# Kernel tuning notes

Hardware: AMD Instinct MI355X
Metric: run time of the kernel (lower is better)

## Reference

```python
import jax, jax.numpy as jnp
import numpy as np

DIM = 1024
HEADS = 16
DIM_HEAD = 64
DIM_INNER = HEADS * DIM_HEAD
SCALE = DIM_HEAD ** -0.5


def rmsnorm(x, w):
    eps = jnp.asarray(jnp.finfo(x.dtype).eps, x.dtype)
    var = jnp.mean(jnp.square(x), axis=-1, keepdims=True)
    return x * jax.lax.rsqrt(var + eps) * w


def setup_inputs() -> dict:
    key = jax.random.key(0)
    ks = jax.random.split(key, 6)
    tokens = jax.random.normal(ks[0], (2, 2048, DIM), dtype=jnp.float32)
    norm_w = jnp.ones((DIM,), dtype=jnp.float32)
    Wq = jax.random.normal(ks[1], (DIM, DIM_INNER), dtype=jnp.float32) * 0.02
    Wkv = jax.random.normal(ks[2], (DIM, 2 * DIM_INNER), dtype=jnp.float32) * 0.02
    Wout = jax.random.normal(ks[3], (DIM_INNER, DIM), dtype=jnp.float32) * 0.02
    Wg = jax.random.normal(ks[4], (DIM, HEADS), dtype=jnp.float32) * 0.02
    return {"tokens": tokens, "norm_w": norm_w, "Wq": Wq, "Wkv": Wkv, "Wout": Wout, "Wg": Wg}


def reference(tokens, norm_w, Wq, Wkv, Wout, Wg):
    b, n, _ = tokens.shape
    x = rmsnorm(tokens, norm_w)                      # [b, n, dim]
    q = x @ Wq                                       # [b, n, h*d]
    kv = x @ Wkv                                     # self-attention: context = tokens
    k, v = jnp.split(kv, 2, axis=-1)

    def split_heads(t):
        return t.reshape(b, n, HEADS, DIM_HEAD).transpose(0, 2, 1, 3)  # [b, h, n, d]

    q, k, v = map(split_heads, (q, k, v))

    sim = jnp.einsum('bhid,bhjd->bhij', q, k) * SCALE  # [b, h, n, n]
    causal_mask = jnp.triu(jnp.ones((n, n), dtype=bool), k=1)
    sim = jnp.where(causal_mask, jnp.asarray(-jnp.finfo(sim.dtype).max, sim.dtype), sim)
    attn = jax.nn.softmax(sim, axis=-1)
    out = jnp.einsum('bhij,bhjd->bhid', attn, v)       # [b, h, n, d]

    gates = jax.nn.sigmoid(x @ Wg)                     # [b, n, h]
    gates = gates.transpose(0, 2, 1)[..., None]        # [b, h, n, 1]
    out = gates * out

    out = out.transpose(0, 2, 1, 3).reshape(b, n, DIM_INNER)  # merge heads
    return out @ Wout                                  # [b, n, dim]
```

## Files before the change

### kernel.cpp

```cpp
#include <hip/hip_runtime.h>
#include <hip/hip_bf16.h>
#include <math.h>

constexpr int BB = 2;
constexpr int NN = 2048;
constexpr int DM = 1024;
constexpr int NH = 16;
constexpr int HD = 64;
constexpr int DI = NH * HD;
constexpr int MT = BB * NN;
constexpr float SM_SCALE = 0.125f * 1.44269504089f;

typedef __attribute__((ext_vector_type(8))) short short8v;
typedef __attribute__((ext_vector_type(4))) float f32x4;

__device__ inline unsigned cvt_pk_bf16(float lo, float hi) {
  unsigned r;
  asm("v_cvt_pk_bf16_f32 %0, %1, %2" : "=v"(r) : "v"(lo), "v"(hi));
  return r;
}
__device__ inline void pl32_swap(unsigned& a, unsigned& b) {
  asm("v_permlane32_swap_b32 %0, %1" : "+v"(a), "+v"(b));
}
__device__ inline void pl16_swap(unsigned& a, unsigned& b) {
  asm("v_permlane16_swap_b32 %0, %1" : "+v"(a), "+v"(b));
}
__device__ __forceinline__ void gload16(const void* g, void* l) {
  __builtin_amdgcn_global_load_lds(
      (const __attribute__((address_space(1))) unsigned int*)g,
      (__attribute__((address_space(3))) unsigned int*)l, 16, 0, 0);
}

__global__ __launch_bounds__(256) void k_rmsnorm(const float* __restrict__ tokens,
                                                 const float* __restrict__ w,
                                                 float* __restrict__ x,
                                                 __hip_bfloat16* __restrict__ xb) {
  const int tok = blockIdx.x;
  const int t = threadIdx.x;
  float4 v = ((const float4*)(tokens + (size_t)tok * DM))[t];
  float ss = v.x * v.x + v.y * v.y + v.z * v.z + v.w * v.w;
#pragma unroll
  for (int m = 1; m < 64; m <<= 1) ss += __shfl_xor(ss, m, 64);
  __shared__ float red[4];
  if ((t & 63) == 0) red[t >> 6] = ss;
  __syncthreads();
  float tot = red[0] + red[1] + red[2] + red[3];
  float inv = rsqrtf(tot * (1.0f / DM) + 1.1920929e-7f);
  float4 wv = ((const float4*)w)[t];
  float4 o;
  o.x = v.x * inv * wv.x;
  o.y = v.y * inv * wv.y;
  o.z = v.z * inv * wv.z;
  o.w = v.w * inv * wv.w;
  ((float4*)(x + (size_t)tok * DM))[t] = o;
  uint2 pk = make_uint2(cvt_pk_bf16(o.x, o.y), cvt_pk_bf16(o.z, o.w));
  *(uint2*)(xb + (size_t)tok * DM + t * 4) = pk;
}

__global__ __launch_bounds__(256) void k_wtrans(const float* __restrict__ W,
                                                __hip_bfloat16* __restrict__ Wt, int N) {
  __shared__ float tile[32][33];
  const int t = threadIdx.x;
  const int c = t & 31, r8 = t >> 5;
  const int kb = blockIdx.y * 32, nb = blockIdx.x * 32;
#pragma unroll
  for (int i = 0; i < 4; i++)
    tile[r8 + i * 8][c] = W[(size_t)(kb + r8 + i * 8) * N + nb + c];
  __syncthreads();
#pragma unroll
  for (int i = 0; i < 4; i++)
    Wt[(size_t)(nb + r8 + i * 8) * DM + kb + c] = __float2bfloat16(tile[c][r8 + i * 8]);
}

template <int MODE>
__global__ __launch_bounds__(256) void k_mgemm(const __hip_bfloat16* __restrict__ A,
                                               const __hip_bfloat16* __restrict__ Bt,
                                               float* __restrict__ C,
                                               __hip_bfloat16* __restrict__ OK,
                                               __hip_bfloat16* __restrict__ OV, int Nc) {
  __shared__ __hip_bfloat16 As[128][32];
  __shared__ __hip_bfloat16 Bs[64][32];
  const int t = threadIdx.x, wid = t >> 6, lane = t & 63;
  const int lq = lane & 15, lg = lane >> 4;
  const int wr = wid >> 1, wc = wid & 1;
  const int m0 = blockIdx.y * 128, n0 = blockIdx.x * 64;
  const int srow = lane >> 2, scol = (lane & 3) * 8;

  const __hip_bfloat16* Ag = A + (size_t)(m0 + wid * 32 + srow) * DM + scol;
  const __hip_bfloat16* Bg = Bt + (size_t)(n0 + wid * 16 + srow) * DM + scol;

  f32x4 acc[4][2];
#pragma unroll
  for (int i = 0; i < 4; i++)
#pragma unroll
    for (int j = 0; j < 2; j++) acc[i][j] = (f32x4){0.f, 0.f, 0.f, 0.f};

  for (int k0 = 0; k0 < DM; k0 += 32) {
    __syncthreads();
    gload16(Ag + k0, &As[wid * 32][0]);
    gload16(Ag + 16 * DM + k0, &As[wid * 32 + 16][0]);
    gload16(Bg + k0, &Bs[wid * 16][0]);
    __syncthreads();
    short8v af[4], bf[2];
#pragma unroll
    for (int i = 0; i < 4; i++) af[i] = *(const short8v*)&As[wr * 64 + i * 16 + lq][lg * 8];
#pragma unroll
    for (int j = 0; j < 2; j++) bf[j] = *(const short8v*)&Bs[wc * 32 + j * 16 + lq][lg * 8];
#pragma unroll
    for (int i = 0; i < 4; i++)
#pragma unroll
      for (int j = 0; j < 2; j++)
        acc[i][j] = __builtin_amdgcn_mfma_f32_16x16x32_bf16(af[i], bf[j], acc[i][j], 0, 0, 0);
  }

#pragma unroll
  for (int i = 0; i < 4; i++) {
    const int mb = m0 + wr * 64 + i * 16 + lg * 4;
#pragma unroll
    for (int j = 0; j < 2; j++) {
      const int c = n0 + wc * 32 + j * 16 + lq;
      if (MODE == 0) {
#pragma unroll
        for (int r = 0; r < 4; r++) C[(size_t)(mb + r) * Nc + c] = acc[i][j][r];
      } else if (MODE == 1 || (MODE == 2 && c < DI)) {
        const int b = mb >> 11, nl = mb & (NN - 1);
        const int h = (c & (DI - 1)) >> 6, d = c & 63;
        __hip_bfloat16* dst = OK + ((size_t)(b * NH + h) * NN + nl) * HD + d;
#pragma unroll
        for (int r = 0; r < 4; r++) dst[(size_t)r * HD] = __float2bfloat16(acc[i][j][r]);
      } else {
        const int cd = c - DI;
        const int b = mb >> 11, nl = mb & (NN - 1);
        const int h = cd >> 6, d = cd & 63;
        uint2 pk = make_uint2(cvt_pk_bf16(acc[i][j][0], acc[i][j][1]),
                              cvt_pk_bf16(acc[i][j][2], acc[i][j][3]));
        *(uint2*)(OV + ((size_t)(b * NH + h) * HD + d) * NN + nl) = pk;
      }
    }
  }
}

__global__ __launch_bounds__(256) void k_gates(const float* __restrict__ x,
                                               const float* __restrict__ Wg,
                                               float* __restrict__ g) {
  const int tok = blockIdx.x * 16 + (threadIdx.x >> 4);
  const int h = threadIdx.x & 15;
  const float* xr = x + (size_t)tok * DM;
  float s = 0.f;
  for (int k = 0; k < DM; k += 4) {
    float4 xv = *(const float4*)(xr + k);
    s += xv.x * Wg[(k + 0) * NH + h];
    s += xv.y * Wg[(k + 1) * NH + h];
    s += xv.z * Wg[(k + 2) * NH + h];
    s += xv.w * Wg[(k + 3) * NH + h];
  }
  g[(size_t)tok * NH + h] = 1.f / (1.f + __expf(-s));
}

__global__ __launch_bounds__(64) void k_attn_mfma(const __hip_bfloat16* __restrict__ Qb,
                                                  const __hip_bfloat16* __restrict__ Kb,
                                                  const __hip_bfloat16* __restrict__ Vtb,
                                                  const float* __restrict__ gates,
                                                  __hip_bfloat16* __restrict__ aob,
                                                  float* __restrict__ Opart,
                                                  float* __restrict__ mpart,
                                                  float* __restrict__ lpart) {
  const int bid = blockIdx.x;
  const int xcd = bid & 7;
  const int s = bid >> 3;
  const int gq = s / 96;
  const int t = s % 96;
  const int bh = gq * 8 + xcd;
  const int i = t / 3, j = t % 3;
  int grp, kt0, kt1, chunk;
  if (j < 2) {
    grp = 63 - i;
    chunk = j;
    const int nt = (grp >> 1) + 1;
    const int h0 = (nt + 1) >> 1;
    kt0 = chunk ? h0 : 0;
    kt1 = chunk ? nt : h0;
  } else {
    grp = 31 - i;
    chunk = -1;
    kt0 = 0;
    kt1 = (grp >> 1) + 1;
  }
  const int lane = threadIdx.x;
  const int lg = lane >> 4, lq = lane & 15;
  const int q0 = grp * 32;

  const __hip_bfloat16* Qh = Qb + (size_t)bh * NN * HD;
  const __hip_bfloat16* Kh = Kb + (size_t)bh * NN * HD;
  const __hip_bfloat16* Vh = Vtb + (size_t)bh * HD * NN;

  short8v qf0[2], qf1[2];
#pragma unroll
  for (int ks = 0; ks < 2; ks++) {
    qf0[ks] = *(const short8v*)(Qh + (size_t)(q0 + lq) * HD + ks * 32 + lg * 8);
    qf1[ks] = *(const short8v*)(Qh + (size_t)(q0 + 16 + lq) * HD + ks * 32 + lg * 8);
  }

  f32x4 oacc0[4], oacc1[4];
#pragma unroll
  for (int jx = 0; jx < 4; jx++) {
    oacc0[jx] = (f32x4){0.f, 0.f, 0.f, 0.f};
    oacc1[jx] = (f32x4){0.f, 0.f, 0.f, 0.f};
  }
  float m0r = -3.0e38f, l0p = 0.f, m1r = -3.0e38f, l1p = 0.f;

  auto LOADK = [&](short8v (*kf)[2], int kt) {
    const int kvb = kt * 64;
#pragma unroll
    for (int jx = 0; jx < 4; jx++)
#pragma unroll
      for (int ks = 0; ks < 2; ks++)
        kf[jx][ks] = *(const short8v*)(Kh + (size_t)(kvb + jx * 16 + lq) * HD + ks * 32 + lg * 8);
  };
  auto LOADV = [&](short8v (*vf)[2], int kt) {
    const int kvb = kt * 64;
#pragma unroll
    for (int jx = 0; jx < 4; jx++)
#pragma unroll
      for (int ks = 0; ks < 2; ks++)
        vf[jx][ks] = *(const short8v*)(Vh + (size_t)(jx * 16 + lq) * NN + kvb + ks * 32 + lg * 8);
  };

  auto GROUP = [&](const short8v* qf, f32x4* oacc, float& m_run, float& l_part,
                   int q0g, const short8v (*kf)[2], const short8v (*vf)[2], int kt) {
    const int kvb = kt * 64;
    f32x4 sacc[4];
#pragma unroll
    for (int jx = 0; jx < 4; jx++) sacc[jx] = (f32x4){0.f, 0.f, 0.f, 0.f};
#pragma unroll
    for (int jx = 0; jx < 4; jx++)
#pragma unroll
      for (int ks = 0; ks < 2; ks++)
        sacc[jx] = __builtin_amdgcn_mfma_f32_16x16x32_bf16(kf[jx][ks], qf[ks], sacc[jx], 0, 0, 0);

    const int qg = q0g + lq;
    const bool diag = (kvb + 63 > q0g);
    float ss[4][4];
#pragma unroll
    for (int jx = 0; jx < 4; jx++)
#pragma unroll
      for (int r = 0; r < 4; r++) {
        float v = sacc[jx][r] * SM_SCALE;
        if (diag && (kvb + jx * 16 + lg * 4 + r > qg)) v = -3.0e38f;
        ss[jx][r] = v;
      }

    float tmax = -3.0e38f;
#pragma unroll
    for (int jx = 0; jx < 4; jx++)
#pragma unroll
      for (int r = 0; r < 4; r++) tmax = fmaxf(tmax, ss[jx][r]);

    if (!__all(tmax <= m_run + 8.0f)) {
      float tr = fmaxf(tmax, __shfl_xor(tmax, 16));
      tr = fmaxf(tr, __shfl_xor(tr, 32));
      const float mnew = fmaxf(m_run, tr);
      const float cf = exp2f(m_run - mnew);
      l_part *= cf;
#pragma unroll
      for (int jx = 0; jx < 4; jx++)
#pragma unroll
        for (int r = 0; r < 4; r++) oacc[jx][r] *= cf;
      m_run = mnew;
    }

    float psum = 0.f;
    unsigned upk[4], vpk[4];
#pragma unroll
    for (int jx = 0; jx < 4; jx++) {
      float p0 = exp2f(ss[jx][0] - m_run), p1 = exp2f(ss[jx][1] - m_run);
      float p2 = exp2f(ss[jx][2] - m_run), p3 = exp2f(ss[jx][3] - m_run);
      psum += (p0 + p1) + (p2 + p3);
      upk[jx] = cvt_pk_bf16(p0, p1);
      vpk[jx] = cvt_pk_bf16(p2, p3);
    }
    l_part += psum;

#pragma unroll
    for (int ks = 0; ks < 2; ks++) {
      unsigned w0 = upk[2 * ks], w2 = upk[2 * ks + 1];
      unsigned w1 = vpk[2 * ks], w3 = vpk[2 * ks + 1];
      pl32_swap(w0, w2);
      pl16_swap(w0, w2);
      pl32_swap(w1, w3);
      pl16_swap(w1, w3);
      int4 bw = make_int4((int)w0, (int)w1, (int)w2, (int)w3);
      short8v pb = __builtin_bit_cast(short8v, bw);
#pragma unroll
      for (int jx = 0; jx < 4; jx++)
        oacc[jx] = __builtin_amdgcn_mfma_f32_16x16x32_bf16(vf[jx][ks], pb, oacc[jx], 0, 0, 0);
    }
  };

  short8v kf[4][2], vf[4][2];
  for (int kt = kt0; kt < kt1; kt++) {
    LOADK(kf, kt);
    LOADV(vf, kt);
    GROUP(qf0, oacc0, m0r, l0p, q0, kf, vf, kt);
    GROUP(qf1, oacc1, m1r, l1p, q0 + 16, kf, vf, kt);
  }

  float l0 = l0p + __shfl_xor(l0p, 16);
  l0 += __shfl_xor(l0, 32);
  float l1 = l1p + __shfl_xor(l1p, 16);
  l1 += __shfl_xor(l1, 32);

  if (chunk >= 0) {
    const int gi = grp - 32;
    const size_t pidx = (size_t)(bh * 32 + gi) * 2 + chunk;
    float* Op = Opart + pidx * 2048;
#pragma unroll
    for (int jx = 0; jx < 4; jx++) {
      *(f32x4*)(Op + lq * 64 + jx * 16 + lg * 4) = oacc0[jx];
      *(f32x4*)(Op + (16 + lq) * 64 + jx * 16 + lg * 4) = oacc1[jx];
    }
    if (lane < 16) {
      mpart[pidx * 32 + lane] = m0r;
      mpart[pidx * 32 + 16 + lane] = m1r;
      lpart[pidx * 32 + lane] = l0;
      lpart[pidx * 32 + 16 + lane] = l1;
    }
    return;
  }

  const int b = bh >> 4, h = bh & 15;
  const float g0 = gates[((size_t)(b * NN + q0 + lq)) * NH + h];
  const float g1 = gates[((size_t)(b * NN + q0 + 16 + lq)) * NH + h];
  const float sc0 = g0 / l0, sc1 = g1 / l1;
  __shared__ float ots[32][68];
#pragma unroll
  for (int jx = 0; jx < 4; jx++)
#pragma unroll
    for (int r = 0; r < 4; r++) {
      ots[lq][jx * 16 + lg * 4 + r] = oacc0[jx][r] * sc0;
      ots[16 + lq][jx * 16 + lg * 4 + r] = oacc1[jx][r] * sc1;
    }
  __syncthreads();
  const int d0 = (lane & 3) * 16;
#pragma unroll
  for (int rr = 0; rr < 2; rr++) {
    const int rl = rr * 16 + (lane >> 2);
    __hip_bfloat16* aor = aob + ((size_t)(b * NN + q0 + rl)) * DI + h * HD + d0;
#pragma unroll
    for (int u = 0; u < 4; u++) {
      uint2 pk = make_uint2(
          cvt_pk_bf16(ots[rl][d0 + 4 * u + 0], ots[rl][d0 + 4 * u + 1]),
          cvt_pk_bf16(ots[rl][d0 + 4 * u + 2], ots[rl][d0 + 4 * u + 3]));
      *(uint2*)(aor + 4 * u) = pk;
    }
  }
}

__global__ __launch_bounds__(256) void k_attn_combine(const float* __restrict__ Opart,
                                                      const float* __restrict__ mpart,
                                                      const float* __restrict__ lpart,
                                                      const float* __restrict__ gates,
                                                      __hip_bfloat16* __restrict__ aob) {
  const int hg = blockIdx.x;
  const int h = hg >> 5, gi = hg & 31;
  const int grp = 32 + gi;
  const int t = threadIdx.x;
  const int row = t >> 3, dq = (t & 7) * 8;
  const size_t p0 = (size_t)hg * 2, p1 = p0 + 1;
  const float m0 = mpart[p0 * 32 + row], m1 = mpart[p1 * 32 + row];
  const float l0 = lpart[p0 * 32 + row], l1 = lpart[p1 * 32 + row];
  const float M = fmaxf(m0, m1);
  const float a0 = exp2f(m0 - M), a1 = exp2f(m1 - M);
  const float L = a0 * l0 + a1 * l1;
  const int b = h >> 4, hh = h & 15;
  const int grow = grp * 32 + row;
  const float sc = gates[((size_t)(b * NN + grow)) * NH + hh] / L;
  const float* O0 = Opart + p0 * 2048 + row * 64 + dq;
  const float* O1 = Opart + p1 * 2048 + row * 64 + dq;
  unsigned pk[4];
#pragma unroll
  for (int u = 0; u < 4; u++) {
    float x0 = (a0 * O0[2 * u + 0] + a1 * O1[2 * u + 0]) * sc;
    float x1 = (a0 * O0[2 * u + 1] + a1 * O1[2 * u + 1]) * sc;
    pk[u] = cvt_pk_bf16(x0, x1);
  }
  __hip_bfloat16* dst = aob + ((size_t)(b * NN + grow)) * DI + hh * 64 + dq;
  *(uint4*)dst = make_uint4(pk[0], pk[1], pk[2], pk[3]);
}

extern "C" void kernel_launch(void* const* d_in, const int* in_sizes, int n_in,
                              void* d_out, int out_size, void* d_ws, size_t ws_size,
                              hipStream_t stream) {
  const float* tokens = (const float*)d_in[0];
  const float* norm_w = (const float*)d_in[1];
  const float* Wq     = (const float*)d_in[2];
  const float* Wkv    = (const float*)d_in[3];
  const float* Wout   = (const float*)d_in[4];
  const float* Wg     = (const float*)d_in[5];
  float* out = (float*)d_out;

  float* ws = (float*)d_ws;
  float* x  = ws;
  float* gb = x + (size_t)MT * DM;
  __hip_bfloat16* xb   = (__hip_bfloat16*)(gb + (size_t)MT * NH);
  __hip_bfloat16* aob  = xb + (size_t)MT * DM;
  __hip_bfloat16* Qb   = aob + (size_t)MT * DM;
  __hip_bfloat16* Kb   = Qb + (size_t)MT * DI;
  __hip_bfloat16* Vtb  = Kb + (size_t)MT * DI;
  __hip_bfloat16* Wqt  = Vtb + (size_t)MT * DI;
  __hip_bfloat16* Wkvt = Wqt + (size_t)DI * DM;
  __hip_bfloat16* Woutt= Wkvt + (size_t)2 * DI * DM;
  float* Opart = (float*)(Woutt + (size_t)DM * DI);
  float* mpart = Opart + (size_t)2048 * 2048;
  float* lpart = mpart + (size_t)2048 * 32;

  k_rmsnorm<<<MT, 256, 0, stream>>>(tokens, norm_w, x, xb);
  k_wtrans<<<dim3(DI / 32, DM / 32), 256, 0, stream>>>(Wq, Wqt, DI);
  k_wtrans<<<dim3(2 * DI / 32, DM / 32), 256, 0, stream>>>(Wkv, Wkvt, 2 * DI);
  k_wtrans<<<dim3(DM / 32, DI / 32), 256, 0, stream>>>(Wout, Woutt, DM);
  k_gates<<<MT / 16, 256, 0, stream>>>(x, Wg, gb);
  k_mgemm<1><<<dim3(DI / 64, MT / 128), 256, 0, stream>>>(xb, Wqt, nullptr, Qb, nullptr, DI);
  k_mgemm<2><<<dim3(2 * DI / 64, MT / 128), 256, 0, stream>>>(xb, Wkvt, nullptr, Kb, Vtb, 2 * DI);
  k_attn_mfma<<<dim3(32 * 96), 64, 0, stream>>>(Qb, Kb, Vtb, gb, aob, Opart, mpart, lpart);
  k_attn_combine<<<dim3(1024), 256, 0, stream>>>(Opart, mpart, lpart, gb, aob);
  k_mgemm<0><<<dim3(DM / 64, MT / 128), 256, 0, stream>>>(aob, Woutt, out, nullptr, nullptr, DM);
}
```

Baseline: 203.2 us.

## Fuse gates into rmsnorm, merge weight transposes and Q/KV GEMMs

Computes the sigmoid gate projection inside the rmsnorm kernel from a shared-memory copy of the normalized row, removing the separate gates kernel and its re-read of x. The three weight-transpose launches become one kernel, and the Q and KV projections run as a single GEMM over a concatenated transposed weight. The goal is fewer launches and a fuller GEMM grid. In exchange, rmsnorm does more work per block and reads Wg with strided loads.

```diff
diff --git a/kernel.cpp b/kernel.cpp
--- a/kernel.cpp
+++ b/kernel.cpp
@@ -33,15 +33,19 @@
 
 __global__ __launch_bounds__(256) void k_rmsnorm(const float* __restrict__ tokens,
                                                  const float* __restrict__ w,
+                                                 const float* __restrict__ Wg,
                                                  float* __restrict__ x,
-                                                 __hip_bfloat16* __restrict__ xb) {
+                                                 __hip_bfloat16* __restrict__ xb,
+                                                 float* __restrict__ g) {
+  __shared__ float xs[DM];
+  __shared__ float red[4];
+  __shared__ float gred[4][16];
   const int tok = blockIdx.x;
   const int t = threadIdx.x;
   float4 v = ((const float4*)(tokens + (size_t)tok * DM))[t];
   float ss = v.x * v.x + v.y * v.y + v.z * v.z + v.w * v.w;
 #pragma unroll
   for (int m = 1; m < 64; m <<= 1) ss += __shfl_xor(ss, m, 64);
-  __shared__ float red[4];
   if ((t & 63) == 0) red[t >> 6] = ss;
   __syncthreads();
   float tot = red[0] + red[1] + red[2] + red[3];
@@ -55,27 +59,58 @@
   ((float4*)(x + (size_t)tok * DM))[t] = o;
   uint2 pk = make_uint2(cvt_pk_bf16(o.x, o.y), cvt_pk_bf16(o.z, o.w));
   *(uint2*)(xb + (size_t)tok * DM + t * 4) = pk;
-}
-
-__global__ __launch_bounds__(256) void k_wtrans(const float* __restrict__ W,
-                                                __hip_bfloat16* __restrict__ Wt, int N) {
+  *(float4*)&xs[t * 4] = o;
+  __syncthreads();
+  const int h = t & 15, seg = t >> 4, wid = t >> 6;
+  const float* xp = &xs[seg * 64];
+  const float* wp = Wg + (size_t)(seg * 64) * NH + h;
+  float s = 0.f;
+#pragma unroll 8
+  for (int k = 0; k < 64; k++) s = fmaf(xp[k], wp[(size_t)k * NH], s);
+  s += __shfl_xor(s, 16);
+  s += __shfl_xor(s, 32);
+  if ((t & 63) < 16) gred[wid][h] = s;
+  __syncthreads();
+  if (t < 16) {
+    float tot2 = gred[0][t] + gred[1][t] + gred[2][t] + gred[3][t];
+    g[(size_t)tok * NH + t] = 1.f / (1.f + __expf(-tot2));
+  }
+}
+
+__global__ __launch_bounds__(256) void k_wtrans_all(const float* __restrict__ Wq,
+                                                    const float* __restrict__ Wkv,
+                                                    const float* __restrict__ Wout,
+                                                    __hip_bfloat16* __restrict__ Wqkvt,
+                                                    __hip_bfloat16* __restrict__ Woutt) {
+  const int bx = blockIdx.x;
+  const int kb = blockIdx.y * 32;
+  const float* W;
+  __hip_bfloat16* dst;
+  int N, col0, drow0;
+  if (bx < 32) {
+    W = Wq; N = DI; col0 = bx * 32; dst = Wqkvt; drow0 = col0;
+  } else if (bx < 96) {
+    W = Wkv; N = 2 * DI; col0 = (bx - 32) * 32; dst = Wqkvt; drow0 = DI + col0;
+  } else {
+    W = Wout; N = DM; col0 = (bx - 96) * 32; dst = Woutt; drow0 = col0;
+  }
   __shared__ float tile[32][33];
   const int t = threadIdx.x;
   const int c = t & 31, r8 = t >> 5;
-  const int kb = blockIdx.y * 32, nb = blockIdx.x * 32;
 #pragma unroll
   for (int i = 0; i < 4; i++)
-    tile[r8 + i * 8][c] = W[(size_t)(kb + r8 + i * 8) * N + nb + c];
+    tile[r8 + i * 8][c] = W[(size_t)(kb + r8 + i * 8) * N + col0 + c];
   __syncthreads();
 #pragma unroll
   for (int i = 0; i < 4; i++)
-    Wt[(size_t)(nb + r8 + i * 8) * DM + kb + c] = __float2bfloat16(tile[c][r8 + i * 8]);
+    dst[(size_t)(drow0 + r8 + i * 8) * DM + kb + c] = __float2bfloat16(tile[c][r8 + i * 8]);
 }
 
 template <int MODE>
 __global__ __launch_bounds__(256) void k_mgemm(const __hip_bfloat16* __restrict__ A,
                                                const __hip_bfloat16* __restrict__ Bt,
                                                float* __restrict__ C,
+                                               __hip_bfloat16* __restrict__ OQ,
                                                __hip_bfloat16* __restrict__ OK,
                                                __hip_bfloat16* __restrict__ OV, int Nc) {
   __shared__ __hip_bfloat16 As[128][32];
@@ -122,39 +157,29 @@
       if (MODE == 0) {
 #pragma unroll
         for (int r = 0; r < 4; r++) C[(size_t)(mb + r) * Nc + c] = acc[i][j][r];
-      } else if (MODE == 1 || (MODE == 2 && c < DI)) {
+      } else {
         const int b = mb >> 11, nl = mb & (NN - 1);
-        const int h = (c & (DI - 1)) >> 6, d = c & 63;
-        __hip_bfloat16* dst = OK + ((size_t)(b * NH + h) * NN + nl) * HD + d;
-#pragma unroll
-        for (int r = 0; r < 4; r++) dst[(size_t)r * HD] = __float2bfloat16(acc[i][j][r]);
-      } else {
-        const int cd = c - DI;
-        const int b = mb >> 11, nl = mb & (NN - 1);
-        const int h = cd >> 6, d = cd & 63;
-        uint2 pk = make_uint2(cvt_pk_bf16(acc[i][j][0], acc[i][j][1]),
-                              cvt_pk_bf16(acc[i][j][2], acc[i][j][3]));
-        *(uint2*)(OV + ((size_t)(b * NH + h) * HD + d) * NN + nl) = pk;
+        if (c < DI) {
+          const int h = c >> 6, d = c & 63;
+          __hip_bfloat16* dst = OQ + ((size_t)(b * NH + h) * NN + nl) * HD + d;
+#pragma unroll
+          for (int r = 0; r < 4; r++) dst[(size_t)r * HD] = __float2bfloat16(acc[i][j][r]);
+        } else if (c < 2 * DI) {
+          const int ck = c - DI;
+          const int h = ck >> 6, d = ck & 63;
+          __hip_bfloat16* dst = OK + ((size_t)(b * NH + h) * NN + nl) * HD + d;
+#pragma unroll
+          for (int r = 0; r < 4; r++) dst[(size_t)r * HD] = __float2bfloat16(acc[i][j][r]);
+        } else {
+          const int cd = c - 2 * DI;
+          const int h = cd >> 6, d = cd & 63;
+          uint2 pk = make_uint2(cvt_pk_bf16(acc[i][j][0], acc[i][j][1]),
+                                cvt_pk_bf16(acc[i][j][2], acc[i][j][3]));
+          *(uint2*)(OV + ((size_t)(b * NH + h) * HD + d) * NN + nl) = pk;
+        }
       }
     }
   }
-}
-
-__global__ __launch_bounds__(256) void k_gates(const float* __restrict__ x,
-                                               const float* __restrict__ Wg,
-                                               float* __restrict__ g) {
-  const int tok = blockIdx.x * 16 + (threadIdx.x >> 4);
-  const int h = threadIdx.x & 15;
-  const float* xr = x + (size_t)tok * DM;
-  float s = 0.f;
-  for (int k = 0; k < DM; k += 4) {
-    float4 xv = *(const float4*)(xr + k);
-    s += xv.x * Wg[(k + 0) * NH + h];
-    s += xv.y * Wg[(k + 1) * NH + h];
-    s += xv.z * Wg[(k + 2) * NH + h];
-    s += xv.w * Wg[(k + 3) * NH + h];
-  }
-  g[(size_t)tok * NH + h] = 1.f / (1.f + __expf(-s));
 }
 
 __global__ __launch_bounds__(64) void k_attn_mfma(const __hip_bfloat16* __restrict__ Qb,
@@ -402,26 +427,23 @@
   float* ws = (float*)d_ws;
   float* x  = ws;
   float* gb = x + (size_t)MT * DM;
-  __hip_bfloat16* xb   = (__hip_bfloat16*)(gb + (size_t)MT * NH);
-  __hip_bfloat16* aob  = xb + (size_t)MT * DM;
-  __hip_bfloat16* Qb   = aob + (size_t)MT * DM;
-  __hip_bfloat16* Kb   = Qb + (size_t)MT * DI;
-  __hip_bfloat16* Vtb  = Kb + (size_t)MT * DI;
-  __hip_bfloat16* Wqt  = Vtb + (size_t)MT * DI;
-  __hip_bfloat16* Wkvt = Wqt + (size_t)DI * DM;
-  __hip_bfloat16* Woutt= Wkvt + (size_t)2 * DI * DM;
+  __hip_bfloat16* xb    = (__hip_bfloat16*)(gb + (size_t)MT * NH);
+  __hip_bfloat16* aob   = xb + (size_t)MT * DM;
+  __hip_bfloat16* Qb    = aob + (size_t)MT * DM;
+  __hip_bfloat16* Kb    = Qb + (size_t)MT * DI;
+  __hip_bfloat16* Vtb   = Kb + (size_t)MT * DI;
+  __hip_bfloat16* Wqkvt = Vtb + (size_t)MT * DI;
+  __hip_bfloat16* Woutt = Wqkvt + (size_t)3 * DI * DM;
   float* Opart = (float*)(Woutt + (size_t)DM * DI);
   float* mpart = Opart + (size_t)2048 * 2048;
   float* lpart = mpart + (size_t)2048 * 32;
 
-  k_rmsnorm<<<MT, 256, 0, stream>>>(tokens, norm_w, x, xb);
-  k_wtrans<<<dim3(DI / 32, DM / 32), 256, 0, stream>>>(Wq, Wqt, DI);
-  k_wtrans<<<dim3(2 * DI / 32, DM / 32), 256, 0, stream>>>(Wkv, Wkvt, 2 * DI);
-  k_wtrans<<<dim3(DM / 32, DI / 32), 256, 0, stream>>>(Wout, Woutt, DM);
-  k_gates<<<MT / 16, 256, 0, stream>>>(x, Wg, gb);
-  k_mgemm<1><<<dim3(DI / 64, MT / 128), 256, 0, stream>>>(xb, Wqt, nullptr, Qb, nullptr, DI);
-  k_mgemm<2><<<dim3(2 * DI / 64, MT / 128), 256, 0, stream>>>(xb, Wkvt, nullptr, Kb, Vtb, 2 * DI);
+  k_rmsnorm<<<MT, 256, 0, stream>>>(tokens, norm_w, Wg, x, xb, gb);
+  k_wtrans_all<<<dim3(128, 32), 256, 0, stream>>>(Wq, Wkv, Wout, Wqkvt, Woutt);
+  k_mgemm<3><<<dim3(3 * DI / 64, MT / 128), 256, 0, stream>>>(
+      xb, Wqkvt, nullptr, Qb, Kb, Vtb, 3 * DI);
   k_attn_mfma<<<dim3(32 * 96), 64, 0, stream>>>(Qb, Kb, Vtb, gb, aob, Opart, mpart, lpart);
   k_attn_combine<<<dim3(1024), 256, 0, stream>>>(Opart, mpart, lpart, gb, aob);
-  k_mgemm<0><<<dim3(DM / 64, MT / 128), 256, 0, stream>>>(aob, Woutt, out, nullptr, nullptr, DM);
-}
+  k_mgemm<0><<<dim3(DM / 64, MT / 128), 256, 0, stream>>>(
+      aob, Woutt, out, nullptr, nullptr, nullptr, DM);
+}
```

Result: faster. 176.3 us (-13.2%).
